# Kernel tuning notes

Hardware: AMD Instinct MI355X
Metric: run time of the kernel (lower is better)

## Reference

```python
import jax, jax.numpy as jnp
import numpy as np

B, T, C, H = 2, 2048, 1024, 16
D = C // H
HID = 4 * C
EPS = 1e-5


def _rmsnorm(x, w):
    return w * (x * jax.lax.rsqrt(jnp.mean(x * x, axis=-1, keepdims=True) + EPS))


def setup_inputs() -> dict:
    key = jax.random.key(0)
    ks = jax.random.split(key, 12)
    s = 0.02
    inp = {
        "x": jax.random.normal(ks[0], (B, T, C), jnp.float32),
        "mask": jnp.tril(jnp.ones((T, T), jnp.int32))[None, None],  # (1,1,T,T) causal
        "attn_norm_w": jnp.ones((C,), jnp.float32),
        "mlp_norm_w": jnp.ones((C,), jnp.float32),
        "q_w": jax.random.normal(ks[1], (C, C), jnp.float32) * s,
        "q_b": jnp.zeros((C,), jnp.float32),
        "k_w": jax.random.normal(ks[2], (C, C), jnp.float32) * s,
        "k_b": jnp.zeros((C,), jnp.float32),
        "v_w": jax.random.normal(ks[3], (C, C), jnp.float32) * s,
        "v_b": jnp.zeros((C,), jnp.float32),
        "o_w": jax.random.normal(ks[4], (C, C), jnp.float32) * s,
        "o_b": jnp.zeros((C,), jnp.float32),
        "w1": jax.random.normal(ks[5], (C, HID), jnp.float32) * s,
        "b1": jnp.zeros((HID,), jnp.float32),
        "w2": jax.random.normal(ks[6], (HID, C), jnp.float32) * s,
        "b2": jnp.zeros((C,), jnp.float32),
    }
    return inp


def reference(x, mask, attn_norm_w, mlp_norm_w, q_w, q_b, k_w, k_b, v_w, v_b,
              o_w, o_b, w1, b1, w2, b2):
    # Pre-norm path (use_post_norm=False)
    h = _rmsnorm(x, attn_norm_w)
    q = (h @ q_w + q_b).reshape(B, T, H, D).transpose(0, 2, 1, 3)  # (B,H,T,D)
    k = (h @ k_w + k_b).reshape(B, T, H, D).transpose(0, 2, 1, 3)
    v = (h @ v_w + v_b).reshape(B, T, H, D).transpose(0, 2, 1, 3)
    scores = jnp.einsum("bhqd,bhkd->bhqk", q, k) / jnp.sqrt(jnp.float32(D))
    scores = jnp.where(mask == 0, jnp.float32(-jnp.inf), scores)
    attn = jax.nn.softmax(scores, axis=-1)  # (B,H,T,T)
    ctx = jnp.einsum("bhqk,bhkd->bhqd", attn, v)
    attn_out = ctx.transpose(0, 2, 1, 3).reshape(B, T, C) @ o_w + o_b
    x = x + attn_out
    m = _rmsnorm(x, mlp_norm_w)
    mlp_out = jax.nn.gelu(m @ w1 + b1, approximate=False) @ w2 + b2
    x = x + mlp_out
    return (x, k, v)
```

## Files before the change

kernel.cpp:

```cpp
#include <hip/hip_runtime.h>
#include <hip/hip_bf16.h>


#define B_ 2
#define T_ 2048
#define C_ 1024
#define H_ 16
#define D_ 64
#define HID_ 4096
#define M_ 4096

typedef __bf16 bf16x8 __attribute__((ext_vector_type(8)));
typedef float f32x4 __attribute__((ext_vector_type(4)));
using bf16 = __hip_bfloat16;

#define WAIT_VM(N) asm volatile("s_waitcnt vmcnt(" #N ")" ::: "memory")
#define SBAR() asm volatile("s_barrier" ::: "memory")

static __device__ __forceinline__ f32x4 mfma16(bf16x8 a, bf16x8 b, f32x4 c) {
  return __builtin_amdgcn_mfma_f32_16x16x32_bf16(a, b, c, 0, 0, 0);
}

static __device__ __forceinline__ void gload16(const bf16* g, bf16* l) {
  __builtin_amdgcn_global_load_lds(
      (const __attribute__((address_space(1))) unsigned int*)g,
      (__attribute__((address_space(3))) unsigned int*)l, 16, 0, 0);
}

static __device__ __forceinline__ unsigned short bfbits(float x) {
  __hip_bfloat16 h = __float2bfloat16(x);
  return *(unsigned short*)&h;
}

__global__ __launch_bounds__(256) void cvt_transpose(const float* __restrict__ in,
                                                     bf16* __restrict__ out, int K, int N) {
  __shared__ float tile[32][33];
  int tid = threadIdx.x, tx = tid & 31, ty = tid >> 5;
  int n0 = blockIdx.x * 32, k0 = blockIdx.y * 32;
#pragma unroll
  for (int i = 0; i < 4; ++i) {
    int r = ty + i * 8;
    tile[r][tx] = in[(size_t)(k0 + r) * N + n0 + tx];
  }
  __syncthreads();
#pragma unroll
  for (int i = 0; i < 4; ++i) {
    int r = ty + i * 8;
    out[(size_t)(n0 + r) * K + k0 + tx] = __float2bfloat16(tile[tx][r]);
  }
}

__global__ __launch_bounds__(256) void pack_bias(const float* __restrict__ q,
                                                 const float* __restrict__ k,
                                                 const float* __restrict__ v,
                                                 float* __restrict__ o) {
  int i = blockIdx.x * 256 + threadIdx.x;
  o[i] = i < 1024 ? q[i] : (i < 2048 ? k[i - 1024] : v[i - 2048]);
}

__global__ __launch_bounds__(256) void rmsnorm_kernel(const float* __restrict__ x,
                                                      const float* __restrict__ w,
                                                      bf16* __restrict__ out) {
  int row = blockIdx.x, tid = threadIdx.x;
  float4 v = ((const float4*)(x + (size_t)row * C_))[tid];
  float ss = v.x * v.x + v.y * v.y + v.z * v.z + v.w * v.w;
#pragma unroll
  for (int d = 1; d < 64; d <<= 1) ss += __shfl_xor(ss, d);
  __shared__ float wsum[4];
  if ((tid & 63) == 0) wsum[tid >> 6] = ss;
  __syncthreads();
  float tot = wsum[0] + wsum[1] + wsum[2] + wsum[3];
  float r = rsqrtf(tot * (1.0f / C_) + 1e-5f);
  float4 wv = ((const float4*)w)[tid];
  bf16* o = out + (size_t)row * C_ + tid * 4;
  o[0] = __float2bfloat16(v.x * wv.x * r);
  o[1] = __float2bfloat16(v.y * wv.y * r);
  o[2] = __float2bfloat16(v.z * wv.z * r);
  o[3] = __float2bfloat16(v.w * wv.w * r);
}

__global__ __launch_bounds__(256) void addp_kernel(float* __restrict__ out,
                                                   const float* __restrict__ p, int n4) {
  int i = blockIdx.x * 256 + threadIdx.x;
  int stride = gridDim.x * 256;
  for (; i < n4; i += stride) {
    float4 a = ((const float4*)out)[i];
    float4 b = ((const float4*)p)[i];
    a.x += b.x; a.y += b.y; a.z += b.z; a.w += b.w;
    ((float4*)out)[i] = a;
  }
}

template <int EPI, int DBUF, int SK>
__global__ __launch_bounds__(256) void gemm_kernel(
    const bf16* __restrict__ A, const bf16* __restrict__ Bt, const float* __restrict__ bias,
    bf16* __restrict__ bfout, float* __restrict__ fout, const float* __restrict__ res,
    bf16* __restrict__ vtb, float* __restrict__ paux, int M, int N, int K) {
  __shared__ bf16 Al[(DBUF ? 2 : 1) * 128 * 64];
  __shared__ bf16 Bl[(DBUF ? 2 : 1) * 128 * 64];
  int tid = threadIdx.x, w = tid >> 6, l = tid & 63;
  int g = l >> 4, c = l & 15;
  int nwg = gridDim.x * gridDim.y;
  int bidl = blockIdx.y * gridDim.x + blockIdx.x;
  int wgid = (bidl & 7) * (nwg >> 3) + (bidl >> 3);
  int bx = wgid % gridDim.x, by = wgid / gridDim.x;
  int m0 = by * 128, n0 = bx * 128;
  int wm = (w >> 1) * 64, wn = (w & 1) * 64;
  int Kc = K / SK;
  int kbase = (SK > 1) ? (int)blockIdx.z * Kc : 0;
  int KT = Kc >> 6;
  int lrow = l >> 3;
  int sgr = (l & 7) ^ lrow;

  const bf16* gA = A + (size_t)(m0 + w * 32 + lrow) * K + kbase + sgr * 8;
  const bf16* gB = Bt + (size_t)(n0 + w * 32 + lrow) * K + kbase + sgr * 8;

  auto stage = [&](int kt, int buf) {
#pragma unroll
    for (int i = 0; i < 4; ++i) {
      gload16(gA + (size_t)i * 8 * K + kt * 64, Al + buf * 8192 + (w * 4 + i) * 512);
      gload16(gB + (size_t)i * 8 * K + kt * 64, Bl + buf * 8192 + (w * 4 + i) * 512);
    }
  };
  auto compute = [&](int buf, f32x4 (&acc)[4][4]) {
#pragma unroll
    for (int ch = 0; ch < 2; ++ch) {
      bf16x8 af[4], bfr[4];
#pragma unroll
      for (int f = 0; f < 4; ++f)
        af[f] = *(const bf16x8*)&Al[buf * 8192 + (wm + f * 16 + c) * 64 +
                                    (((ch * 4 + g) ^ (c & 7)) << 3)];
#pragma unroll
      for (int f = 0; f < 4; ++f)
        bfr[f] = *(const bf16x8*)&Bl[buf * 8192 + (wn + f * 16 + c) * 64 +
                                     (((ch * 4 + g) ^ (c & 7)) << 3)];
#pragma unroll
      for (int mf = 0; mf < 4; ++mf)
#pragma unroll
        for (int nf = 0; nf < 4; ++nf) acc[mf][nf] = mfma16(af[mf], bfr[nf], acc[mf][nf]);
    }
  };

  f32x4 acc[4][4] = {};
  if (DBUF) {
    stage(0, 0);
    for (int kt = 0; kt < KT; ++kt) {
      int cur = kt & 1;
      if (kt + 1 < KT) {
        stage(kt + 1, cur ^ 1);
        WAIT_VM(8);
      } else {
        WAIT_VM(0);
      }
      SBAR();
      __builtin_amdgcn_s_setprio(1);
      compute(cur, acc);
      __builtin_amdgcn_s_setprio(0);
      __builtin_amdgcn_sched_barrier(0);
      SBAR();
    }
  } else {
    for (int kt = 0; kt < KT; ++kt) {
      stage(kt, 0);
      __syncthreads();
      compute(0, acc);
      __syncthreads();
    }
  }

#pragma unroll
  for (int mf = 0; mf < 4; ++mf) {
#pragma unroll
    for (int nf = 0; nf < 4; ++nf) {
      int gn = n0 + wn + nf * 16 + c;
      float bv = bias ? bias[gn] : 0.f;
#pragma unroll
      for (int r = 0; r < 4; ++r) {
        int gm = m0 + wm + mf * 16 + g * 4 + r;
        float vr = acc[mf][nf][r];
        float v = vr + bv;
        if (SK > 1 && blockIdx.z > 0) {
          paux[(size_t)gm * N + gn] = vr;
        } else if (EPI == 0) {
          int part = gn >> 10, wi = gn & 1023, hh = wi >> 6, d = wi & 63;
          int b_ = gm >> 11, t = gm & 2047;
          size_t idx = ((size_t)(b_ * H_ + hh) * T_ + t) * D_ + d;
          if (part == 2) {
            vtb[((size_t)(b_ * H_ + hh) * D_ + d) * T_ + t] = __float2bfloat16(v);
            fout[(size_t)2 * 4194304 + idx] = v;
          } else {
            bfout[(size_t)part * 4194304 + idx] = __float2bfloat16(v);
            if (part) fout[(size_t)part * 4194304 + idx] = v;
          }
        } else if (EPI == 1) {
          size_t idx = (size_t)gm * N + gn;
          fout[idx] = v + res[idx];
        } else {
          size_t idx = (size_t)gm * N + gn;
          float gl = 0.5f * v * (1.0f + erff(v * 0.70710678118f));
          bfout[idx] = __float2bfloat16(gl);
        }
      }
    }
  }
}

__global__ __launch_bounds__(256, 2) void attn_kernel(const bf16* __restrict__ Q,
                                                      const bf16* __restrict__ Kb,
                                                      const bf16* __restrict__ Vt,
                                                      bf16* __restrict__ ctx) {
  constexpr int LDP = 72;
  __shared__ bf16 Kl[2][64 * 64];
  __shared__ bf16 Vl[2][64 * 64];
  __shared__ bf16 Pl[4][2][16 * LDP];
  __shared__ float alw[4][2][16];
  int tid = threadIdx.x, w = tid >> 6, l = tid & 63, g = l >> 4, c = l & 15;
  int bid = blockIdx.x;
  int qt = 15 - (bid >> 5);
  int bh = bid & 31;
  int qbase = qt * 128 + w * 32;
  const bf16* Qh = Q + (size_t)bh * T_ * D_;
  const bf16* Kh = Kb + (size_t)bh * T_ * D_;
  const bf16* Vh = Vt + (size_t)bh * T_ * D_;

  int srow = l >> 3;
  int sce = ((l & 7) * 8) ^ (srow << 3);
  int cswz = (c & 7) << 3;

  auto stage = [&](int ti, int buf) {
#pragma unroll
    for (int i = 0; i < 2; ++i) {
      int row = i * 32 + w * 8 + srow;
      gload16(&Kh[(size_t)(ti * 64 + row) * D_ + sce], &Kl[buf][i * 2048 + w * 512]);
      gload16(&Vh[(size_t)row * T_ + ti * 64 + sce], &Vl[buf][i * 2048 + w * 512]);
    }
  };

  int NT = 2 * qt + 2;
  stage(0, 0);

  bf16x8 aq[2][2];
#pragma unroll
  for (int qf = 0; qf < 2; ++qf)
#pragma unroll
    for (int ch = 0; ch < 2; ++ch)
      aq[qf][ch] = *(const bf16x8*)&Qh[(size_t)(qbase + qf * 16 + c) * D_ + ch * 32 + g * 8];

  f32x4 o[2][4] = {};
  float mrun[2] = {-1e30f, -1e30f};
  float lrun[2] = {0.f, 0.f};

  __syncthreads();

  for (int ti = 0; ti < NT; ++ti) {
    int cur = ti & 1;
    int kv0 = ti * 64;
    if (ti + 1 < NT) stage(ti + 1, cur ^ 1);

    f32x4 sf[2][4];
#pragma unroll
    for (int kb = 0; kb < 4; ++kb) {
      bf16x8 bk0 = *(const bf16x8*)&Kl[cur][(kb * 16 + c) * 64 + ((g * 8) ^ cswz)];
      bf16x8 bk1 = *(const bf16x8*)&Kl[cur][(kb * 16 + c) * 64 + ((32 + g * 8) ^ cswz)];
#pragma unroll
      for (int qf = 0; qf < 2; ++qf) {
        f32x4 t = {};
        t = mfma16(bk0, aq[qf][0], t);
        t = mfma16(bk1, aq[qf][1], t);
        sf[qf][kb] = t;
      }
    }

    float s[2][4][4];
#pragma unroll
    for (int qf = 0; qf < 2; ++qf)
#pragma unroll
      for (int kb = 0; kb < 4; ++kb)
#pragma unroll
        for (int r = 0; r < 4; ++r) s[qf][kb][r] = sf[qf][kb][r] * 0.125f;
    if (kv0 + 63 > qbase) {
#pragma unroll
      for (int qf = 0; qf < 2; ++qf)
#pragma unroll
        for (int kb = 0; kb < 4; ++kb)
#pragma unroll
          for (int r = 0; r < 4; ++r) {
            int qi = qbase + qf * 16 + c;
            int kv = kv0 + kb * 16 + g * 4 + r;
            if (kv > qi) s[qf][kb][r] = -1e30f;
          }
    }

#pragma unroll
    for (int qf = 0; qf < 2; ++qf) {
      float m01 = fmaxf(fmaxf(s[qf][0][0], s[qf][0][1]), fmaxf(s[qf][0][2], s[qf][0][3]));
      float m23 = fmaxf(fmaxf(s[qf][1][0], s[qf][1][1]), fmaxf(s[qf][1][2], s[qf][1][3]));
      float m45 = fmaxf(fmaxf(s[qf][2][0], s[qf][2][1]), fmaxf(s[qf][2][2], s[qf][2][3]));
      float m67 = fmaxf(fmaxf(s[qf][3][0], s[qf][3][1]), fmaxf(s[qf][3][2], s[qf][3][3]));
      float tm = fmaxf(fmaxf(m01, m23), fmaxf(m45, m67));
      tm = fmaxf(tm, __shfl_xor(tm, 16));
      tm = fmaxf(tm, __shfl_xor(tm, 32));
      float mn = fmaxf(mrun[qf], tm);
      float al = __expf(mrun[qf] - mn);
      mrun[qf] = mn;
      float asum = 0.f;
#pragma unroll
      for (int kb = 0; kb < 4; ++kb)
#pragma unroll
        for (int r = 0; r < 4; ++r) {
          float pv = __expf(s[qf][kb][r] - mn);
          s[qf][kb][r] = pv;
          asum += pv;
        }
      asum += __shfl_xor(asum, 16);
      asum += __shfl_xor(asum, 32);
      lrun[qf] = lrun[qf] * al + asum;
      if (l < 16) alw[w][qf][c] = al;
    }

#pragma unroll
    for (int qf = 0; qf < 2; ++qf)
#pragma unroll
      for (int kb = 0; kb < 4; ++kb) {
        union { unsigned short u[4]; uint2 v2; } pk;
#pragma unroll
        for (int r = 0; r < 4; ++r) pk.u[r] = bfbits(s[qf][kb][r]);
        *(uint2*)&Pl[w][qf][c * LDP + kb * 16 + g * 4] = pk.v2;
      }

#pragma unroll
    for (int qf = 0; qf < 2; ++qf) {
      f32x4 a4 = *(const f32x4*)&alw[w][qf][g * 4];
#pragma unroll
      for (int db = 0; db < 4; ++db)
#pragma unroll
        for (int r = 0; r < 4; ++r) o[qf][db][r] *= a4[r];
    }

    bf16x8 bvv[4][2];
#pragma unroll
    for (int db = 0; db < 4; ++db)
#pragma unroll
      for (int ck = 0; ck < 2; ++ck)
        bvv[db][ck] = *(const bf16x8*)&Vl[cur][(db * 16 + c) * 64 + ((ck * 32 + g * 8) ^ cswz)];

#pragma unroll
    for (int qf = 0; qf < 2; ++qf) {
      bf16x8 pa0 = *(const bf16x8*)&Pl[w][qf][c * LDP + g * 8];
      bf16x8 pa1 = *(const bf16x8*)&Pl[w][qf][c * LDP + 32 + g * 8];
#pragma unroll
      for (int db = 0; db < 4; ++db) {
        o[qf][db] = mfma16(pa0, bvv[db][0], o[qf][db]);
        o[qf][db] = mfma16(pa1, bvv[db][1], o[qf][db]);
      }
    }
    __syncthreads();
  }

#pragma unroll
  for (int qf = 0; qf < 2; ++qf)
    if (l < 16) alw[w][qf][c] = 1.0f / lrun[qf];
  int b_ = bh >> 4, hh = bh & 15;
#pragma unroll
  for (int qf = 0; qf < 2; ++qf) {
    f32x4 i4 = *(const f32x4*)&alw[w][qf][g * 4];
#pragma unroll
    for (int r = 0; r < 4; ++r)
#pragma unroll
      for (int db = 0; db < 4; ++db)
        ctx[(size_t)(b_ * T_ + qbase + qf * 16 + g * 4 + r) * C_ + hh * D_ + db * 16 + c] =
            __float2bfloat16(o[qf][db][r] * i4[r]);
  }
}

extern "C" void kernel_launch(void* const* d_in, const int* in_sizes, int n_in, void* d_out,
                              int out_size, void* d_ws, size_t ws_size, hipStream_t stream) {
  const float* x = (const float*)d_in[0];
  const float* anw = (const float*)d_in[2];
  const float* mnw = (const float*)d_in[3];
  const float* q_w = (const float*)d_in[4];
  const float* q_b = (const float*)d_in[5];
  const float* k_w = (const float*)d_in[6];
  const float* k_b = (const float*)d_in[7];
  const float* v_w = (const float*)d_in[8];
  const float* v_b = (const float*)d_in[9];
  const float* o_w = (const float*)d_in[10];
  const float* o_b = (const float*)d_in[11];
  const float* w1 = (const float*)d_in[12];
  const float* b1 = (const float*)d_in[13];
  const float* w2 = (const float*)d_in[14];
  const float* b2 = (const float*)d_in[15];
  float* out = (float*)d_out;
  char* ws = (char*)d_ws;

  bf16* qkvT = (bf16*)(ws + 0);
  bf16* owT = (bf16*)(ws + 6291456);
  bf16* w1T = (bf16*)(ws + 8388608);
  bf16* w2T = (bf16*)(ws + 16777216);
  bf16* h = (bf16*)(ws + 25165824);
  bf16* qb = (bf16*)(ws + 33554432);
  bf16* kb = (bf16*)(ws + 41943040);
  bf16* vtb = (bf16*)(ws + 58720256);
  bf16* ctx = (bf16*)(ws + 67108864);
  float* x2 = (float*)(ws + 33554432);
  bf16* m = h;
  bf16* hid = (bf16*)(ws + 50331648);
  float* qkvb = (float*)(ws + 75497472);
  float* p1 = (float*)(ws + 0);

  cvt_transpose<<<dim3(32, 32), 256, 0, stream>>>(q_w, qkvT, 1024, 1024);
  cvt_transpose<<<dim3(32, 32), 256, 0, stream>>>(k_w, qkvT + 1048576, 1024, 1024);
  cvt_transpose<<<dim3(32, 32), 256, 0, stream>>>(v_w, qkvT + 2097152, 1024, 1024);
  cvt_transpose<<<dim3(32, 32), 256, 0, stream>>>(o_w, owT, 1024, 1024);
  cvt_transpose<<<dim3(128, 32), 256, 0, stream>>>(w1, w1T, 1024, 4096);
  cvt_transpose<<<dim3(32, 128), 256, 0, stream>>>(w2, w2T, 4096, 1024);
  pack_bias<<<12, 256, 0, stream>>>(q_b, k_b, v_b, qkvb);

  rmsnorm_kernel<<<4096, 256, 0, stream>>>(x, anw, h);

  gemm_kernel<0, 1, 1><<<dim3(24, 32), 256, 0, stream>>>(h, qkvT, qkvb, qb, out, nullptr,
                                                         vtb, nullptr, 4096, 3072, 1024);

  attn_kernel<<<512, 256, 0, stream>>>(qb, kb, vtb, ctx);

  gemm_kernel<1, 1, 1><<<dim3(8, 32), 256, 0, stream>>>(ctx, owT, o_b, nullptr, x2, x,
                                                        nullptr, nullptr, 4096, 1024, 1024);

  rmsnorm_kernel<<<4096, 256, 0, stream>>>(x2, mnw, m);

  gemm_kernel<2, 1, 1><<<dim3(32, 32), 256, 0, stream>>>(m, w1T, b1, hid, nullptr, nullptr,
                                                         nullptr, nullptr, 4096, 4096, 1024);
  gemm_kernel<1, 1, 2><<<dim3(8, 32, 2), 256, 0, stream>>>(hid, w2T, b2, nullptr, out, x2,
                                                           nullptr, p1, 4096, 1024, 4096);
  addp_kernel<<<2048, 256, 0, stream>>>(out, p1, 1048576);
}
```

Measured before the change: 301.7 us.

## Split attention KV range across blocks, merge partials, fuse MLP residual via atomics

Attention now launches two blocks per query tile, each covering half of the KV tiles. Each writes unnormalized outputs plus running max and sum, and a new merge kernel combines them into ctx. This targets load imbalance and low occupancy. The output projection epilogue pre-writes x2+b2 into the output, so the split-K down-projection can atomically add its partials, removing the separate add kernel. Exact erf GELU is replaced by a tanh-based approximation, which changes numerics slightly.

```diff
diff --git a/kernel.cpp b/kernel.cpp
--- a/kernel.cpp
+++ b/kernel.cpp
@@ -30,6 +30,15 @@
 static __device__ __forceinline__ unsigned short bfbits(float x) {
   __hip_bfloat16 h = __float2bfloat16(x);
   return *(unsigned short*)&h;
+}
+
+static __device__ __forceinline__ float gelu_tanh(float v) {
+  float z = 0.7978845608f * (v + 0.044715f * v * v * v);
+  float az = fabsf(z);
+  float e = __expf(-2.0f * az);
+  float th = (1.0f - e) / (1.0f + e);
+  th = copysignf(th, z);
+  return 0.5f * v * (1.0f + th);
 }
 
 __global__ __launch_bounds__(256) void cvt_transpose(const float* __restrict__ in,
@@ -79,23 +88,12 @@
   o[3] = __float2bfloat16(v.w * wv.w * r);
 }
 
-__global__ __launch_bounds__(256) void addp_kernel(float* __restrict__ out,
-                                                   const float* __restrict__ p, int n4) {
-  int i = blockIdx.x * 256 + threadIdx.x;
-  int stride = gridDim.x * 256;
-  for (; i < n4; i += stride) {
-    float4 a = ((const float4*)out)[i];
-    float4 b = ((const float4*)p)[i];
-    a.x += b.x; a.y += b.y; a.z += b.z; a.w += b.w;
-    ((float4*)out)[i] = a;
-  }
-}
-
 template <int EPI, int DBUF, int SK>
 __global__ __launch_bounds__(256) void gemm_kernel(
     const bf16* __restrict__ A, const bf16* __restrict__ Bt, const float* __restrict__ bias,
     bf16* __restrict__ bfout, float* __restrict__ fout, const float* __restrict__ res,
-    bf16* __restrict__ vtb, float* __restrict__ paux, int M, int N, int K) {
+    bf16* __restrict__ vtb, float* __restrict__ paux, const float* __restrict__ bias2,
+    int M, int N, int K) {
   __shared__ bf16 Al[(DBUF ? 2 : 1) * 128 * 64];
   __shared__ bf16 Bl[(DBUF ? 2 : 1) * 128 * 64];
   int tid = threadIdx.x, w = tid >> 6, l = tid & 63;
@@ -179,7 +177,9 @@
         int gm = m0 + wm + mf * 16 + g * 4 + r;
         float vr = acc[mf][nf][r];
         float v = vr + bv;
-        if (SK > 1 && blockIdx.z > 0) {
+        if (EPI == 4) {
+          atomicAdd(fout + (size_t)gm * N + gn, vr);
+        } else if (SK > 1 && blockIdx.z > 0) {
           paux[(size_t)gm * N + gn] = vr;
         } else if (EPI == 0) {
           int part = gn >> 10, wi = gn & 1023, hh = wi >> 6, d = wi & 63;
@@ -192,13 +192,14 @@
             bfout[(size_t)part * 4194304 + idx] = __float2bfloat16(v);
             if (part) fout[(size_t)part * 4194304 + idx] = v;
           }
-        } else if (EPI == 1) {
+        } else if (EPI == 3) {
           size_t idx = (size_t)gm * N + gn;
-          fout[idx] = v + res[idx];
+          float t = v + res[idx];
+          fout[idx] = t;
+          paux[idx] = t + bias2[gn];
         } else {
           size_t idx = (size_t)gm * N + gn;
-          float gl = 0.5f * v * (1.0f + erff(v * 0.70710678118f));
-          bfout[idx] = __float2bfloat16(gl);
+          bfout[idx] = __float2bfloat16(gelu_tanh(v));
         }
       }
     }
@@ -208,7 +209,9 @@
 __global__ __launch_bounds__(256, 2) void attn_kernel(const bf16* __restrict__ Q,
                                                       const bf16* __restrict__ Kb,
                                                       const bf16* __restrict__ Vt,
-                                                      bf16* __restrict__ ctx) {
+                                                      bf16* __restrict__ o0p,
+                                                      bf16* __restrict__ o1p,
+                                                      float* __restrict__ ml) {
   constexpr int LDP = 72;
   __shared__ bf16 Kl[2][64 * 64];
   __shared__ bf16 Vl[2][64 * 64];
@@ -216,13 +219,18 @@
   __shared__ float alw[4][2][16];
   int tid = threadIdx.x, w = tid >> 6, l = tid & 63, g = l >> 4, c = l & 15;
   int bid = blockIdx.x;
-  int qt = 15 - (bid >> 5);
   int bh = bid & 31;
+  int rest = bid >> 5;
+  int qt = 15 - (rest >> 1);
+  int half = rest & 1;
   int qbase = qt * 128 + w * 32;
   const bf16* Qh = Q + (size_t)bh * T_ * D_;
   const bf16* Kh = Kb + (size_t)bh * T_ * D_;
   const bf16* Vh = Vt + (size_t)bh * T_ * D_;
 
+  int NT = 2 * qt + 2, H0 = qt + 1;
+  int t0 = half ? H0 : 0, t1 = half ? NT : H0;
+
   int srow = l >> 3;
   int sce = ((l & 7) * 8) ^ (srow << 3);
   int cswz = (c & 7) << 3;
@@ -236,8 +244,7 @@
     }
   };
 
-  int NT = 2 * qt + 2;
-  stage(0, 0);
+  stage(t0, 0);
 
   bf16x8 aq[2][2];
 #pragma unroll
@@ -252,10 +259,10 @@
 
   __syncthreads();
 
-  for (int ti = 0; ti < NT; ++ti) {
-    int cur = ti & 1;
+  for (int ti = t0; ti < t1; ++ti) {
+    int cur = (ti - t0) & 1;
     int kv0 = ti * 64;
-    if (ti + 1 < NT) stage(ti + 1, cur ^ 1);
+    if (ti + 1 < t1) stage(ti + 1, cur ^ 1);
 
     f32x4 sf[2][4];
 #pragma unroll
@@ -287,7 +294,7 @@
           for (int r = 0; r < 4; ++r) {
             int qi = qbase + qf * 16 + c;
             int kv = kv0 + kb * 16 + g * 4 + r;
-            if (kv > qi) s[qf][kb][r] = -1e30f;
+            if (kv > qi) s[qf][kb][r] = -3.0e38f;
           }
     }
 
@@ -357,19 +364,47 @@
     __syncthreads();
   }
 
+  bf16* op = half ? o1p : o0p;
+  int rowbase = bh * 2048 + qbase;
 #pragma unroll
   for (int qf = 0; qf < 2; ++qf)
-    if (l < 16) alw[w][qf][c] = 1.0f / lrun[qf];
+#pragma unroll
+    for (int r = 0; r < 4; ++r)
+#pragma unroll
+      for (int db = 0; db < 4; ++db)
+        op[(size_t)(rowbase + qf * 16 + g * 4 + r) * 64 + db * 16 + c] =
+            __float2bfloat16(o[qf][db][r]);
+  if (l < 16) {
+    float* mh = ml + half * 131072;
+#pragma unroll
+    for (int qf = 0; qf < 2; ++qf) {
+      mh[rowbase + qf * 16 + c] = mrun[qf];
+      mh[65536 + rowbase + qf * 16 + c] = lrun[qf];
+    }
+  }
+}
+
+__global__ __launch_bounds__(256) void merge_attn(const bf16* __restrict__ o0,
+                                                  const bf16* __restrict__ o1,
+                                                  const float* __restrict__ ml,
+                                                  bf16* __restrict__ ctx) {
+  int idx = blockIdx.x * 256 + threadIdx.x;
+  int row = idx >> 2, dc = (idx & 3) * 16;
+  float m0 = ml[row], l0 = ml[65536 + row];
+  float m1 = ml[131072 + row], l1 = ml[196608 + row];
+  float Mx = fmaxf(m0, m1);
+  float s0 = __expf(m0 - Mx), s1 = __expf(m1 - Mx);
+  float inv = 1.0f / (l0 * s0 + l1 * s1);
+  const bf16x8* p0 = (const bf16x8*)&o0[(size_t)row * 64 + dc];
+  const bf16x8* p1 = (const bf16x8*)&o1[(size_t)row * 64 + dc];
+  bf16x8 a0 = p0[0], a1 = p0[1], b0 = p1[0], b1 = p1[1];
+  int bh = row >> 11, t = row & 2047;
   int b_ = bh >> 4, hh = bh & 15;
-#pragma unroll
-  for (int qf = 0; qf < 2; ++qf) {
-    f32x4 i4 = *(const f32x4*)&alw[w][qf][g * 4];
-#pragma unroll
-    for (int r = 0; r < 4; ++r)
-#pragma unroll
-      for (int db = 0; db < 4; ++db)
-        ctx[(size_t)(b_ * T_ + qbase + qf * 16 + g * 4 + r) * C_ + hh * D_ + db * 16 + c] =
-            __float2bfloat16(o[qf][db][r] * i4[r]);
+  bf16* dst = ctx + ((size_t)(b_ * T_ + t)) * C_ + hh * D_ + dc;
+#pragma unroll
+  for (int j = 0; j < 8; ++j) {
+    dst[j] = __float2bfloat16(((float)a0[j] * s0 + (float)b0[j] * s1) * inv);
+    dst[8 + j] = __float2bfloat16(((float)a1[j] * s0 + (float)b1[j] * s1) * inv);
   }
 }
 
@@ -400,13 +435,15 @@
   bf16* h = (bf16*)(ws + 25165824);
   bf16* qb = (bf16*)(ws + 33554432);
   bf16* kb = (bf16*)(ws + 41943040);
+  bf16* o0p = (bf16*)(ws + 50331648);
   bf16* vtb = (bf16*)(ws + 58720256);
   bf16* ctx = (bf16*)(ws + 67108864);
+  bf16* o1p = (bf16*)(ws + 75497472);
+  float* ml = (float*)(ws + 25165824);
   float* x2 = (float*)(ws + 33554432);
   bf16* m = h;
   bf16* hid = (bf16*)(ws + 50331648);
   float* qkvb = (float*)(ws + 75497472);
-  float* p1 = (float*)(ws + 0);
 
   cvt_transpose<<<dim3(32, 32), 256, 0, stream>>>(q_w, qkvT, 1024, 1024);
   cvt_transpose<<<dim3(32, 32), 256, 0, stream>>>(k_w, qkvT + 1048576, 1024, 1024);
@@ -418,19 +455,19 @@
 
   rmsnorm_kernel<<<4096, 256, 0, stream>>>(x, anw, h);
 
-  gemm_kernel<0, 1, 1><<<dim3(24, 32), 256, 0, stream>>>(h, qkvT, qkvb, qb, out, nullptr,
-                                                         vtb, nullptr, 4096, 3072, 1024);
-
-  attn_kernel<<<512, 256, 0, stream>>>(qb, kb, vtb, ctx);
-
-  gemm_kernel<1, 1, 1><<<dim3(8, 32), 256, 0, stream>>>(ctx, owT, o_b, nullptr, x2, x,
-                                                        nullptr, nullptr, 4096, 1024, 1024);
+  gemm_kernel<0, 1, 1><<<dim3(24, 32), 256, 0, stream>>>(
+      h, qkvT, qkvb, qb, out, nullptr, vtb, nullptr, nullptr, 4096, 3072, 1024);
+
+  attn_kernel<<<1024, 256, 0, stream>>>(qb, kb, vtb, o0p, o1p, ml);
+  merge_attn<<<1024, 256, 0, stream>>>(o0p, o1p, ml, ctx);
+
+  gemm_kernel<3, 1, 1><<<dim3(8, 32), 256, 0, stream>>>(
+      ctx, owT, o_b, nullptr, x2, x, nullptr, out, b2, 4096, 1024, 1024);
 
   rmsnorm_kernel<<<4096, 256, 0, stream>>>(x2, mnw, m);
 
-  gemm_kernel<2, 1, 1><<<dim3(32, 32), 256, 0, stream>>>(m, w1T, b1, hid, nullptr, nullptr,
-                                                         nullptr, nullptr, 4096, 4096, 1024);
-  gemm_kernel<1, 1, 2><<<dim3(8, 32, 2), 256, 0, stream>>>(hid, w2T, b2, nullptr, out, x2,
-                                                           nullptr, p1, 4096, 1024, 4096);
-  addp_kernel<<<2048, 256, 0, stream>>>(out, p1, 1048576);
-}
+  gemm_kernel<2, 1, 1><<<dim3(32, 32), 256, 0, stream>>>(
+      m, w1T, b1, hid, nullptr, nullptr, nullptr, nullptr, nullptr, 4096, 4096, 1024);
+  gemm_kernel<4, 1, 2><<<dim3(8, 32, 2), 256, 0, stream>>>(
+      hid, w2T, nullptr, nullptr, out, nullptr, nullptr, nullptr, nullptr, 4096, 1024, 4096);
+}
```

After: 280.0 us. 1.08x faster.
